# Kernel tuning notes

Measured on AMD Instinct MI355X. Metric: run time of the kernel, lower is better.

Reference implementation:

```python
import jax, jax.numpy as jnp
import numpy as np
import math

B, U, IN, H = 4096, 6, 256, 600
IKS, IVS, NIH = 64, 400, 1           # input attention key/value sizes, heads
CKS, CQS, NCH = 32, 32, 4            # comm attention key/query sizes, heads
CVS = H                              # comm value size forced to hidden_size
K = 4                                # top-k active units


@jax.custom_vjp
def blocked_grad(x, mask):
    return x

def _bg_fwd(x, mask):
    return x, mask

def _bg_bwd(mask, g):
    return (g * mask, jnp.zeros_like(mask))

blocked_grad.defvjp(_bg_fwd, _bg_bwd)


def _gll(x, w):
    # GroupLinearLayer: per-unit bmm, x (B,U,din) @ w (U,din,dout) -> (B,U,dout)
    return jnp.einsum('bud,udo->buo', x, w)


def setup_inputs() -> dict:
    key = jax.random.key(0)
    ks = jax.random.split(key, 16)
    r = lambda i, shape: (0.02 * jax.random.normal(ks[i], shape)).astype(jnp.float32)
    return dict(
        x=jax.random.normal(ks[0], (B, 1, IN), jnp.float32),
        hs=jax.random.normal(ks[1], (B, U, H), jnp.float32),
        Wk=r(2, (IN, NIH * IKS)), bk=jnp.zeros((NIH * IKS,), jnp.float32),
        Wv=r(3, (IN, NIH * IVS)), bv=jnp.zeros((NIH * IVS,), jnp.float32),
        Wq=r(4, (U, H, NIH * IKS)),
        x2h_w=r(5, (U, IVS, 3 * H)), h2h_w=r(6, (U, H, 3 * H)),
        Wq_=r(7, (U, H, NCH * CQS)), Wk_=r(8, (U, H, NCH * CKS)),
        Wv_=r(9, (U, H, NCH * CVS)), Wout=r(10, (U, NCH * CVS, CVS)),
    )


def reference(x, hs, Wk, bk, Wv, bv, Wq, x2h_w, h2h_w, Wq_, Wk_, Wv_, Wout):
    h_old = hs
    # append null input along dim 1 -> (B,2,IN)
    xcat = jnp.concatenate([x, jnp.zeros_like(x)], axis=1)
    # ---- input attention + top-k mask ----
    key_l = (xcat @ Wk + bk).reshape(B, 2, NIH, IKS).transpose(0, 2, 1, 3)   # (B,1,2,ks)
    val_l = (xcat @ Wv + bv).reshape(B, 2, NIH, IVS).mean(axis=2)             # (B,2,vs) mean over heads
    qry_l = _gll(hs, Wq).reshape(B, U, NIH, IKS).transpose(0, 2, 1, 3)        # (B,1,U,ks)
    scores = jnp.einsum('bhuk,bhnk->bhun', qry_l, key_l) / math.sqrt(IKS)
    scores = scores.mean(axis=1)                                               # (B,U,2)
    not_null = scores[:, :, 0]
    _, idx = jax.lax.top_k(not_null, K)                                        # (B,K)
    mask = jnp.zeros((B, U), jnp.float32).at[jnp.arange(B)[:, None], idx].set(1.0)
    probs = jax.nn.softmax(scores, axis=-1)                                    # dropout is identity (eval)
    inputs = jnp.einsum('bun,bnv->buv', probs, val_l) * mask[:, :, None]       # (B,U,vs)
    # ---- GroupGRU cell ----
    gx = _gll(inputs, x2h_w)
    gh = _gll(hs, h2h_w)
    i_r, i_i, i_n = jnp.split(gx, 3, axis=2)
    h_r, h_i, h_n = jnp.split(gh, 3, axis=2)
    rg = jax.nn.sigmoid(i_r + h_r)
    ig = jax.nn.sigmoid(i_i + h_i)
    ng = jnp.tanh(i_n + rg * h_n)
    hs = ng + ig * (hs - ng)
    # ---- communication attention (with blocked_grad) ----
    h_b = blocked_grad(hs, mask[:, :, None])
    q = _gll(h_b, Wq_).reshape(B, U, NCH, CQS).transpose(0, 2, 1, 3)   # (B,4,U,32)
    k = _gll(h_b, Wk_).reshape(B, U, NCH, CKS).transpose(0, 2, 1, 3)
    v = _gll(h_b, Wv_).reshape(B, U, NCH, CVS).transpose(0, 2, 1, 3)   # (B,4,U,600)
    att = jax.nn.softmax(jnp.einsum('bhuk,bhnk->bhun', q, k) / math.sqrt(CKS), axis=-1)
    att = att * mask[:, None, :, None]   # zero rows of inactive query units
    ctx = jnp.einsum('bhun,bhnv->bhuv', att, v).transpose(0, 2, 1, 3).reshape(B, U, NCH * CVS)
    ctx = _gll(ctx, Wout) + h_b
    m = mask[:, :, None]
    return m * ctx + (1.0 - m) * h_old
```

## Files before the change

kernel.cpp:

```cpp
#include <hip/hip_runtime.h>
#include <math.h>

typedef unsigned short u16;
typedef __attribute__((ext_vector_type(8))) short short8;
typedef __attribute__((ext_vector_type(4))) float f32x4;

constexpr int NB   = 4096;
constexpr int NU   = 6;
constexpr int NIN  = 256;
constexpr int NH   = 600;
constexpr int IKS  = 64;
constexpr int IVS  = 400;
constexpr int NCH  = 4;
constexpr int CVS  = 600;
constexpr int KTOP = 4;

constexpr int KVW  = IKS + IVS;
constexpr int QKW  = 256;
constexpr int VW   = NCH * CVS;

constexpr int KGRU = 1024;
constexpr int HOFS = 416;
constexpr int NGATE = 640;
constexpr int KH   = 640;
constexpr int VN   = 2432;
constexpr int BC   = 1024;
constexpr int NCHUNK = NB / BC;

constexpr long OFF_KV   = 0;
constexpr long OFF_QRY  = OFF_KV   + (long)NB * KVW;
constexpr long OFF_C0   = OFF_QRY  + (long)NB * NU * IKS;
constexpr long OFF_C1   = OFF_C0   + (long)NB * NU;
constexpr long OFF_MASK = OFF_C1   + (long)NB * NU;
constexpr long OFF_QK   = OFF_MASK + (long)NB * NU;
constexpr long OFF_ATTW = OFF_QK   + (long)NB * NU * QKW;
constexpr long OFF_HNBF = OFF_ATTW + (long)NB * NCH * NU * NU;
constexpr long OFF_WQK  = OFF_HNBF + (long)NU * NB * KH / 2;
constexpr long OFF_WV   = OFF_WQK  + (long)NU * QKW * KH / 2;
constexpr long OFF_WOUT = OFF_WV   + (long)NU * VN * KH / 2;
constexpr long OFF_WGRU = OFF_WOUT + (long)NU * NGATE * VN / 2;
constexpr long OFF_AGRU = OFF_WGRU + (long)NU * 3 * NGATE * KGRU / 2;
constexpr long OFF_VBUF = OFF_WGRU;
constexpr long OFF_CTXB = OFF_VBUF + (long)BC * NU * VN / 2;

__device__ __forceinline__ u16 f2bf(float f) {
    unsigned int x = __float_as_uint(f);
    x += 0x7FFFu + ((x >> 16) & 1u);
    return (u16)(x >> 16);
}
__device__ __forceinline__ float bf2f(u16 u) {
    return __uint_as_float(((unsigned int)u) << 16);
}
__device__ __forceinline__ void gl_lds16(const u16* g, u16* l) {
    __builtin_amdgcn_global_load_lds(
        (const __attribute__((address_space(1))) void*)g,
        (__attribute__((address_space(3))) void*)l, 16, 0, 0);
}

#define WAITVM_(N) asm volatile("s_waitcnt vmcnt(" #N ")" ::: "memory")
#define WAITVM(N)  WAITVM_(N)
#define WAITLG()   asm volatile("s_waitcnt lgkmcnt(0)" ::: "memory")
#define SBAR()     do { __builtin_amdgcn_sched_barrier(0); \
                        __builtin_amdgcn_s_barrier();      \
                        __builtin_amdgcn_sched_barrier(0); } while (0)

__global__ __launch_bounds__(256)
void wtrans_kernel(const float* __restrict__ src, long s_u, int s_ld, int s_colofs,
                   int Ksrc, int Nsub,
                   u16* __restrict__ dst, long d_u, int d_ld, int d_nofs, int d_kofs,
                   int gdiv, int s_gcol, int d_gnofs)
{
    __shared__ float tile[32][33];
    int z = blockIdx.z;
    int u = z, g = 0;
    if (gdiv > 1) { u = z / gdiv; g = z % gdiv; }
    const int k0 = blockIdx.x * 32, n0 = blockIdx.y * 32;
    const int t  = threadIdx.x;
    const int scol = s_colofs + g * s_gcol;
    const int dnof = d_nofs + g * d_gnofs;
    const float* S = src + (long)u * s_u;
    u16* D = dst + (long)u * d_u;
    #pragma unroll
    for (int r = 0; r < 4; r++) {
        int kk = r * 8 + (t >> 5), nn = t & 31;
        float v = 0.f;
        if (k0 + kk < Ksrc && n0 + nn < Nsub)
            v = S[(long)(k0 + kk) * s_ld + scol + n0 + nn];
        tile[kk][nn] = v;
    }
    __syncthreads();
    #pragma unroll
    for (int r = 0; r < 4; r++) {
        int nn = r * 8 + (t >> 5), kk = t & 31;
        if (n0 + nn < Nsub)
            D[(long)(dnof + n0 + nn) * d_ld + d_kofs + k0 + kk] = f2bf(tile[kk][nn]);
    }
}

__global__ __launch_bounds__(256)
void gemm_kv_kernel(const float* __restrict__ x,
                    const float* __restrict__ Wk, const float* __restrict__ bk,
                    const float* __restrict__ Wv, const float* __restrict__ bv,
                    float* __restrict__ kvout)
{
    const int m0 = blockIdx.x * 64;
    const int n0 = blockIdx.y * 64;
    const int tid = threadIdx.x;
    const int tm = tid / 16, tn = tid % 16;
    constexpr int K = NIN, N = KVW;

    __shared__ __align__(16) float As[32][72];
    __shared__ __align__(16) float Ws[32][68];
    float acc[4][4] = {};

    for (int k0 = 0; k0 < K; k0 += 32) {
        #pragma unroll
        for (int s2 = 0; s2 < 2; s2++) {
            int s = tid * 2 + s2;
            int row = s >> 3, kc = s & 7;
            float4 v = *(const float4*)&x[(long)(m0 + row) * K + k0 + kc * 4];
            As[kc*4+0][row] = v.x; As[kc*4+1][row] = v.y;
            As[kc*4+2][row] = v.z; As[kc*4+3][row] = v.w;
        }
        #pragma unroll
        for (int s2 = 0; s2 < 2; s2++) {
            int s = tid * 2 + s2;
            int kr = s >> 4, c4 = s & 15;
            int cg = n0 + c4 * 4;
            float4 v = {0,0,0,0};
            if (cg < IKS)    v = *(const float4*)&Wk[(long)(k0+kr)*IKS + cg];
            else if (cg < N) v = *(const float4*)&Wv[(long)(k0+kr)*IVS + (cg - IKS)];
            *(float4*)&Ws[kr][c4*4] = v;
        }
        __syncthreads();
        #pragma unroll
        for (int kk = 0; kk < 32; kk++) {
            float4 a4 = *(const float4*)&As[kk][tm*4];
            float4 w4 = *(const float4*)&Ws[kk][tn*4];
            float av[4] = {a4.x,a4.y,a4.z,a4.w}, wv[4] = {w4.x,w4.y,w4.z,w4.w};
            #pragma unroll
            for (int i = 0; i < 4; i++)
                #pragma unroll
                for (int j = 0; j < 4; j++)
                    acc[i][j] = fmaf(av[i], wv[j], acc[i][j]);
        }
        __syncthreads();
    }
    #pragma unroll
    for (int i = 0; i < 4; i++) {
        int row = m0 + tm*4 + i;
        #pragma unroll
        for (int j = 0; j < 4; j++) {
            int cg = n0 + tn*4 + j;
            if (cg < N) {
                float bias = (cg < IKS) ? bk[cg] : bv[cg - IKS];
                kvout[(long)row*N + cg] = acc[i][j] + bias;
            }
        }
    }
}

__global__ __launch_bounds__(256)
void gemm_qry_kernel(const float* __restrict__ A,
                     const float* __restrict__ W,
                     float* __restrict__ C)
{
    const int u  = blockIdx.z;
    const int m0 = blockIdx.x * 64;
    const int tid = threadIdx.x;
    const int tm = tid / 16, tn = tid % 16;
    constexpr int K = NH, N = IKS;
    const long lda = (long)NU * NH;

    __shared__ __align__(16) float As[32][72];
    __shared__ __align__(16) float Ws[32][68];
    const float* Au = A + (long)u * K;
    const float* Wu = W + (long)u * K * N;
    float acc[4][4] = {};

    for (int k0 = 0; k0 < K; k0 += 32) {
        #pragma unroll
        for (int s2 = 0; s2 < 2; s2++) {
            int s = tid * 2 + s2;
            int row = s >> 3, kc = s & 7;
            float4 v = {0,0,0,0};
            if (k0 + kc*4 < K)
                v = *(const float4*)&Au[(long)(m0 + row) * lda + k0 + kc * 4];
            As[kc*4+0][row] = v.x; As[kc*4+1][row] = v.y;
            As[kc*4+2][row] = v.z; As[kc*4+3][row] = v.w;
        }
        #pragma unroll
        for (int s2 = 0; s2 < 2; s2++) {
            int s = tid * 2 + s2;
            int kr = s >> 4, c4 = s & 15;
            float4 v = {0,0,0,0};
            if (k0 + kr < K)
                v = *(const float4*)&Wu[(long)(k0 + kr) * N + c4 * 4];
            *(float4*)&Ws[kr][c4*4] = v;
        }
        __syncthreads();
        #pragma unroll
        for (int kk = 0; kk < 32; kk++) {
            float4 a4 = *(const float4*)&As[kk][tm*4];
            float4 w4 = *(const float4*)&Ws[kk][tn*4];
            float av[4] = {a4.x,a4.y,a4.z,a4.w}, wv[4] = {w4.x,w4.y,w4.z,w4.w};
            #pragma unroll
            for (int i = 0; i < 4; i++)
                #pragma unroll
                for (int j = 0; j < 4; j++)
                    acc[i][j] = fmaf(av[i], wv[j], acc[i][j]);
        }
        __syncthreads();
    }
    #pragma unroll
    for (int i = 0; i < 4; i++) {
        int row = m0 + tm*4 + i;
        #pragma unroll
        for (int j = 0; j < 4; j++) {
            int c = tn*4 + j;
            C[(long)row*(NU*IKS) + (long)u*IKS + c] = acc[i][j];
        }
    }
}

__global__ __launch_bounds__(64)
void score_kernel(const float* __restrict__ qry, const float* __restrict__ kv,
                  const float* __restrict__ bk,
                  float* __restrict__ c0, float* __restrict__ c1,
                  float* __restrict__ maskf)
{
    const int b = blockIdx.x;
    const int t = threadIdx.x;
    __shared__ float s0s[NU], s1s[NU];

    float k0v = kv[(long)b*KVW + t];
    float bkv = bk[t];
    for (int u = 0; u < NU; u++) {
        float q  = qry[((long)b*NU + u)*IKS + t];
        float p0 = q * k0v, p1 = q * bkv;
        #pragma unroll
        for (int off = 32; off > 0; off >>= 1) {
            p0 += __shfl_down(p0, off);
            p1 += __shfl_down(p1, off);
        }
        if (t == 0) { s0s[u] = p0 * 0.125f; s1s[u] = p1 * 0.125f; }
    }
    __syncthreads();
    if (t < NU) {
        int u = t;
        float su = s0s[u];
        int rank = 0;
        #pragma unroll
        for (int j = 0; j < NU; j++) {
            float sj = s0s[j];
            if (sj > su || (sj == su && j < u)) rank++;
        }
        float m = (rank < KTOP) ? 1.0f : 0.0f;
        float a = s0s[u], bb = s1s[u];
        float mx = fmaxf(a, bb);
        float e0 = expf(a - mx), e1 = expf(bb - mx);
        float p0 = e0 / (e0 + e1);
        c0[(long)b*NU + u]    = m * p0;
        c1[(long)b*NU + u]    = m * (1.0f - p0);
        maskf[(long)b*NU + u] = m;
    }
}

__global__ __launch_bounds__(256)
void prep_gruA_kernel(const float* __restrict__ kv, const float* __restrict__ bv,
                      const float* __restrict__ hs,
                      const float* __restrict__ c0, const float* __restrict__ c1,
                      u16* __restrict__ Ag)
{
    long id = (long)blockIdx.x * 256 + threadIdx.x;
    const long total = (long)NU * NB * (KGRU / 8);
    if (id >= total) return;
    int k8 = (int)(id % (KGRU / 8));
    int b  = (int)((id / (KGRU / 8)) % NB);
    int u  = (int)(id / ((long)(KGRU / 8) * NB));
    int k  = k8 * 8;
    u16 o[8];
    if (k < IVS) {
        float cv0 = c0[(long)b*NU + u], cv1 = c1[(long)b*NU + u];
        const float* kp = kv + (long)b*KVW + IKS + k;
        const float* bp = bv + k;
        #pragma unroll
        for (int i = 0; i < 8; i++) o[i] = f2bf(cv0*kp[i] + cv1*bp[i]);
    } else if (k >= HOFS && k < HOFS + NH) {
        const float* hp = hs + ((long)b*NU + u)*NH + (k - HOFS);
        #pragma unroll
        for (int i = 0; i < 8; i++) o[i] = f2bf(hp[i]);
    } else {
        #pragma unroll
        for (int i = 0; i < 8; i++) o[i] = 0;
    }
    *(short8*)&Ag[id * 8] = *(const short8*)o;
}

__global__ __launch_bounds__(256, 3)
void gru_mfma_kernel(const u16* __restrict__ Ag, const u16* __restrict__ Wg,
                     const float* __restrict__ hs, u16* __restrict__ hnbf)
{
    const int u  = blockIdx.z;
    const int m0 = blockIdx.x * 128;
    const int n0 = blockIdx.y * 32;
    const int tid = threadIdx.x;
    const int wid = tid >> 6, lane = tid & 63;
    const int wm = wid >> 1, wn = wid & 1;
    const int lrow = lane & 15, lkq = lane >> 4;
    const int srow = lane >> 2;
    const int scs  = (((lane & 3) ^ ((lane >> 3) & 3)) * 8);
    const int cofs = ((lkq ^ ((lrow >> 1) & 3)) * 8);

    __shared__ __align__(16) u16 As[3][128 * 32];
    __shared__ __align__(16) u16 Bs[3][128 * 32];

    const u16* Au = Ag + (long)u * NB * KGRU;
    const u16* Wu = Wg + (long)u * 3 * NGATE * KGRU;

    f32x4 aR[4], aI[4], aNX[4], aNH[4];
    #pragma unroll
    for (int m = 0; m < 4; m++) {
        aR[m] = (f32x4){0,0,0,0}; aI[m] = (f32x4){0,0,0,0};
        aNX[m] = (f32x4){0,0,0,0}; aNH[m] = (f32x4){0,0,0,0};
    }

#define GSTAGE(BUF, T) do {                                                   \
        const long kk0 = (long)(T) * 32;                                      \
        _Pragma("unroll")                                                     \
        for (int i2 = 0; i2 < 2; i2++) {                                      \
            int R = wid*32 + i2*16;                                           \
            int row = R + srow;                                               \
            gl_lds16(Au + (long)(m0 + row)*KGRU + kk0 + scs,                  \
                     &As[BUF][R * 32]);                                       \
            int g = row >> 5; if (g > 2) g = 2;     \
            int rn = row & 31;                                                \
            gl_lds16(Wu + ((long)g*NGATE + n0 + rn)*KGRU + kk0 + scs,         \
                     &Bs[BUF][R * 32]);                                       \
        }                                                                     \
    } while (0)

#define GCOMPUTE(BUF, T) do {                                                 \
        __builtin_amdgcn_s_setprio(1);                                        \
        short8 af[4], bR, bI, bN;                                             \
        _Pragma("unroll")                                                     \
        for (int m = 0; m < 4; m++)                                           \
            af[m] = *(const short8*)&As[BUF][(wm*64 + m*16 + lrow)*32 + cofs];\
        {                                                                     \
            int nr = wn*16 + lrow;                                            \
            bR = *(const short8*)&Bs[BUF][(0*32 + nr)*32 + cofs];             \
            bI = *(const short8*)&Bs[BUF][(1*32 + nr)*32 + cofs];             \
            bN = *(const short8*)&Bs[BUF][(2*32 + nr)*32 + cofs];             \
        }                                                                     \
        _Pragma("unroll")                                                     \
        for (int m = 0; m < 4; m++) {                                         \
            aR[m] = __builtin_amdgcn_mfma_f32_16x16x32_bf16(af[m], bR, aR[m], 0, 0, 0); \
            aI[m] = __builtin_amdgcn_mfma_f32_16x16x32_bf16(af[m], bI, aI[m], 0, 0, 0); \
        }                                                                     \
        if ((T) < HOFS/32) {                                                  \
            _Pragma("unroll")                                                 \
            for (int m = 0; m < 4; m++)                                       \
                aNX[m] = __builtin_amdgcn_mfma_f32_16x16x32_bf16(af[m], bN, aNX[m], 0, 0, 0); \
        } else {                                                              \
            _Pragma("unroll")                                                 \
            for (int m = 0; m < 4; m++)                                       \
                aNH[m] = __builtin_amdgcn_mfma_f32_16x16x32_bf16(af[m], bN, aNH[m], 0, 0, 0); \
        }                                                                     \
        __builtin_amdgcn_s_setprio(0);                                        \
    } while (0)

    constexpr int KSTEPS = KGRU / 32;
    GSTAGE(0, 0);
    int bc = 0, bn = 1;
    for (int t = 0; t < KSTEPS - 1; ++t) {
        GSTAGE(bn, t + 1);
        WAITVM(4); SBAR();
        GCOMPUTE(bc, t);
        bc = bn; bn = (bn == 2) ? 0 : bn + 1;
    }
    WAITVM(0); SBAR();
    GCOMPUTE(bc, KSTEPS - 1);
#undef GCOMPUTE
#undef GSTAGE

    #pragma unroll
    for (int m = 0; m < 4; m++) {
        #pragma unroll
        for (int r = 0; r < 4; r++) {
            int row = m0 + wm*64 + m*16 + lkq*4 + r;
            int col = n0 + wn*16 + lrow;
            u16 ov = 0;
            if (col < NH) {
                float rg = 1.0f / (1.0f + expf(-aR[m][r]));
                float ig = 1.0f / (1.0f + expf(-aI[m][r]));
                float ng = tanhf(aNX[m][r] + rg * aNH[m][r]);
                float h  = hs[((long)row*NU + u)*NH + col];
                ov = f2bf(ng + ig * (h - ng));
            }
            hnbf[(long)u*NB*KH + (long)row*KH + col] = ov;
        }
    }
}

template<int EPI>
__global__ __launch_bounds__(256, 2)
void mfgemm_kernel(const u16* __restrict__ A, long sAu, int lda,
                   const u16* __restrict__ Bw, long sBu, int ldb,
                   float* __restrict__ Cf, u16* __restrict__ C16,
                   long sCu, int ldc, int ksteps,
                   const float* __restrict__ maskf,
                   const u16* __restrict__ hnbf,
                   const float* __restrict__ hs,
                   int bbase)
{
    const int u  = blockIdx.z;
    const int m0 = blockIdx.x * 128;
    const int n0 = blockIdx.y * 128;
    const int tid = threadIdx.x;
    const int wid = tid >> 6, lane = tid & 63;
    const int wm = wid >> 1, wn = wid & 1;
    const int lrow = lane & 15, lkq = lane >> 4;
    const int l8 = lane & 7, lr8 = lane >> 3;
    const int rsw = lrow & 7;

    __shared__ __align__(16) u16 As[2][128 * 64];
    __shared__ __align__(16) u16 Bs[2][128 * 64];

    const u16* Au = A + (long)u * sAu;
    const u16* Bu = Bw + (long)u * sBu;

    f32x4 acc[4][4];
    #pragma unroll
    for (int m = 0; m < 4; m++)
        #pragma unroll
        for (int n = 0; n < 4; n++) acc[m][n] = (f32x4){0,0,0,0};

#define MSTAGE(BUF, KS) do {                                                  \
        const long kk0 = (long)(KS) * 64;                                     \
        _Pragma("unroll")                                                     \
        for (int i2 = 0; i2 < 4; i2++) {                                      \
            int rw = i2*32 + wid*8 + lr8;                                     \
            int co = ((l8 ^ (rw & 7)) * 8);                                   \
            gl_lds16(Au + (long)(m0 + rw)*lda + kk0 + co,                     \
                     &As[BUF][(i2*32 + wid*8) * 64]);                         \
            gl_lds16(Bu + (long)(n0 + rw)*ldb + kk0 + co,                     \
                     &Bs[BUF][(i2*32 + wid*8) * 64]);                         \
        }                                                                     \
    } while (0)

#define MCOMPUTE(BUF) do {                                                    \
        __builtin_amdgcn_s_setprio(1);                                        \
        _Pragma("unroll")                                                     \
        for (int ks2 = 0; ks2 < 2; ks2++) {                                   \
            const int cofs = (((ks2*4 + lkq) ^ rsw) * 8);                     \
            short8 af[4], bfr[4];                                             \
            _Pragma("unroll")                                                 \
            for (int m = 0; m < 4; m++)                                       \
                af[m] = *(const short8*)&As[BUF][(wm*64 + m*16 + lrow)*64 + cofs]; \
            _Pragma("unroll")                                                 \
            for (int n = 0; n < 4; n++)                                       \
                bfr[n] = *(const short8*)&Bs[BUF][(wn*64 + n*16 + lrow)*64 + cofs]; \
            _Pragma("unroll")                                                 \
            for (int m = 0; m < 4; m++)                                       \
                _Pragma("unroll")                                             \
                for (int n = 0; n < 4; n++)                                   \
                    acc[m][n] = __builtin_amdgcn_mfma_f32_16x16x32_bf16(af[m], bfr[n], acc[m][n], 0, 0, 0); \
        }                                                                     \
        __builtin_amdgcn_s_setprio(0);                                        \
    } while (0)

#define MPH(BUF, T, W) do {                                                   \
        if ((T) + 1 < ksteps) MSTAGE((BUF)^1, (T)+1);                         \
        WAITVM(W); SBAR();                                                    \
        MCOMPUTE(BUF);                                                        \
        WAITLG(); SBAR();                                                     \
    } while (0)

    MSTAGE(0, 0);
    int t = 0;
    for (; t + 2 < ksteps; t += 2) { MPH(0, t, 8); MPH(1, t+1, 8); }
    if (t + 2 == ksteps) { MPH(0, t, 8); MPH(1, t+1, 0); }
    else                 { MPH(0, t, 0); }
#undef MPH
#undef MCOMPUTE
#undef MSTAGE

    #pragma unroll
    for (int m = 0; m < 4; m++) {
        #pragma unroll
        for (int r = 0; r < 4; r++) {
            int row = m0 + wm*64 + m*16 + lkq*4 + r;
            #pragma unroll
            for (int n = 0; n < 4; n++) {
                int col = n0 + wn*64 + n*16 + lrow;
                float v = acc[m][n][r];
                if (EPI == 0) {
                    Cf[(long)u*sCu + (long)row*ldc + col] = v;
                } else if (EPI == 2) {
                    C16[(long)u*sCu + (long)row*ldc + col] = f2bf(v);
                } else {
                    if (col < NH) {
                        int b = bbase + row;
                        long o = ((long)b*NU + u)*NH + col;
                        float mk = maskf[(long)b*NU + u];
                        float hv = bf2f(hnbf[(long)u*NB*KH + (long)b*KH + col]);
                        Cf[o] = (mk > 0.5f) ? (v + hv) : hs[o];
                    }
                }
            }
        }
    }
}

__global__ __launch_bounds__(64)
void attw_kernel(const float* __restrict__ qk, const float* __restrict__ maskf,
                 float* __restrict__ attw)
{
    const int bh = blockIdx.x;
    const int b = bh / NCH, h = bh % NCH;
    const int t = threadIdx.x;
    __shared__ float lg[NU][NU];

    if (t < NU * NU) {
        int uq = t / NU, un = t % NU;
        const float* qp = qk + ((long)b*NU + uq)*QKW + h*32;
        const float* kp = qk + ((long)b*NU + un)*QKW + 128 + h*32;
        float s = 0;
        #pragma unroll
        for (int i = 0; i < 32; i++) s = fmaf(qp[i], kp[i], s);
        lg[uq][un] = s * 0.17677669529663687f;
    }
    __syncthreads();
    if (t < NU) {
        int uq = t;
        float mx = -1e30f;
        #pragma unroll
        for (int n = 0; n < NU; n++) mx = fmaxf(mx, lg[uq][n]);
        float e[NU], se = 0;
        #pragma unroll
        for (int n = 0; n < NU; n++) { e[n] = expf(lg[uq][n] - mx); se += e[n]; }
        float m = maskf[(long)b*NU + uq];
        float inv = m / se;
        #pragma unroll
        for (int n = 0; n < NU; n++)
            attw[(((long)b*NCH + h)*NU + uq)*NU + n] = e[n] * inv;
    }
}

__global__ __launch_bounds__(256)
void ctx2_kernel(const float* __restrict__ attw, const u16* __restrict__ v16,
                 u16* __restrict__ ctx16, int bbase)
{
    __shared__ float att_s[32][NCH * NU * NU];
    const int c0 = blockIdx.x * 64;
    const int b0 = blockIdx.y * 32;
    const int tid = threadIdx.x;

    for (int i = tid; i < 32 * 144; i += 256) {
        int bl = i / 144, j = i % 144;
        att_s[bl][j] = attw[(long)(bbase + b0 + bl) * 144 + j];
    }
    __syncthreads();

    const int bl = tid >> 3;
    const int c  = c0 + (tid & 7) * 8;
    const long rowbase = (long)(b0 + bl) * NU;

    if (c >= VW) {
        short8 z = {0,0,0,0,0,0,0,0};
        #pragma unroll
        for (int u = 0; u < NU; u++)
            *(short8*)&ctx16[(rowbase + u) * VN + c] = z;
        return;
    }
    const int h = c / CVS;
    const float* aw = &att_s[bl][h * 36];

    float acc[NU][8] = {};
    #pragma unroll
    for (int n = 0; n < NU; n++) {
        short8 vv = *(const short8*)&v16[(rowbase + n) * VN + c];
        float vf[8];
        #pragma unroll
        for (int i = 0; i < 8; i++) vf[i] = bf2f((u16)vv[i]);
        #pragma unroll
        for (int u = 0; u < NU; u++) {
            float a = aw[u * 6 + n];
            #pragma unroll
            for (int i = 0; i < 8; i++) acc[u][i] = fmaf(a, vf[i], acc[u][i]);
        }
    }
    #pragma unroll
    for (int u = 0; u < NU; u++) {
        short8 o;
        #pragma unroll
        for (int i = 0; i < 8; i++) o[i] = (short)f2bf(acc[u][i]);
        *(short8*)&ctx16[(rowbase + u) * VN + c] = o;
    }
}

extern "C" void kernel_launch(void* const* d_in, const int* in_sizes, int n_in,
                              void* d_out, int out_size, void* d_ws, size_t ws_size,
                              hipStream_t stream)
{
    const float* x    = (const float*)d_in[0];
    const float* hs   = (const float*)d_in[1];
    const float* Wk   = (const float*)d_in[2];
    const float* bk   = (const float*)d_in[3];
    const float* Wv   = (const float*)d_in[4];
    const float* bv   = (const float*)d_in[5];
    const float* Wq   = (const float*)d_in[6];
    const float* x2h  = (const float*)d_in[7];
    const float* h2h  = (const float*)d_in[8];
    const float* Wq_  = (const float*)d_in[9];
    const float* Wk_  = (const float*)d_in[10];
    const float* Wv_  = (const float*)d_in[11];
    const float* Wout = (const float*)d_in[12];
    float* out = (float*)d_out;
    float* ws  = (float*)d_ws;

    float* kv    = ws + OFF_KV;
    float* qry   = ws + OFF_QRY;
    float* c0b   = ws + OFF_C0;
    float* c1b   = ws + OFF_C1;
    float* maskf = ws + OFF_MASK;
    float* qk    = ws + OFF_QK;
    float* attw  = ws + OFF_ATTW;
    u16*   hnbf  = (u16*)(ws + OFF_HNBF);
    u16*   wqk   = (u16*)(ws + OFF_WQK);
    u16*   wv    = (u16*)(ws + OFF_WV);
    u16*   wout  = (u16*)(ws + OFF_WOUT);
    u16*   wgru  = (u16*)(ws + OFF_WGRU);
    u16*   agru  = (u16*)(ws + OFF_AGRU);
    u16*   vbuf16 = (u16*)(ws + OFF_VBUF);
    u16*   ctx16  = (u16*)(ws + OFF_CTXB);

    wtrans_kernel<<<dim3(20, 4, NU), 256, 0, stream>>>(
        Wq_, (long)NH*128, 128, 0, NH, 128, wqk, (long)QKW*KH, KH, 0, 0, 1, 0, 0);
    wtrans_kernel<<<dim3(20, 4, NU), 256, 0, stream>>>(
        Wk_, (long)NH*128, 128, 0, NH, 128, wqk, (long)QKW*KH, KH, 128, 0, 1, 0, 0);
    wtrans_kernel<<<dim3(20, 75, NU), 256, 0, stream>>>(
        Wv_, (long)NH*VW, VW, 0, NH, VW, wv, (long)VN*KH, KH, 0, 0, 1, 0, 0);
    wtrans_kernel<<<dim3(76, 19, NU), 256, 0, stream>>>(
        Wout, (long)VW*NH, NH, 0, VW, NH, wout, (long)NGATE*VN, VN, 0, 0, 1, 0, 0);
    wtrans_kernel<<<dim3(13, 19, NU*3), 256, 0, stream>>>(
        x2h, (long)IVS*3*NH, 3*NH, 0, IVS, NH,
        wgru, (long)3*NGATE*KGRU, KGRU, 0, 0, 3, NH, NGATE);
    wtrans_kernel<<<dim3(19, 19, NU*3), 256, 0, stream>>>(
        h2h, (long)NH*3*NH, 3*NH, 0, NH, NH,
        wgru, (long)3*NGATE*KGRU, KGRU, 0, HOFS, 3, NH, NGATE);

    gemm_kv_kernel<<<dim3(NB/64, (KVW+63)/64), 256, 0, stream>>>(x, Wk, bk, Wv, bv, kv);
    gemm_qry_kernel<<<dim3(NB/64, 1, NU), 256, 0, stream>>>(hs, Wq, qry);
    score_kernel<<<NB, 64, 0, stream>>>(qry, kv, bk, c0b, c1b, maskf);

    {
        long total = (long)NU * NB * (KGRU/8);
        prep_gruA_kernel<<<(unsigned)((total + 255)/256), 256, 0, stream>>>(
            kv, bv, hs, c0b, c1b, agru);
    }
    gru_mfma_kernel<<<dim3(NB/128, NGATE/32, NU), 256, 0, stream>>>(agru, wgru, hs, hnbf);

    mfgemm_kernel<0><<<dim3(NB/128, QKW/128, NU), 256, 0, stream>>>(
        hnbf, (long)NB*KH, KH, wqk, (long)QKW*KH, KH,
        qk, nullptr, (long)QKW, NU*QKW, KH/64, nullptr, nullptr, nullptr, 0);
    attw_kernel<<<NB*NCH, 64, 0, stream>>>(qk, maskf, attw);

    for (int ch = 0; ch < NCHUNK; ch++) {
        mfgemm_kernel<2><<<dim3(BC/128, VN/128, NU), 256, 0, stream>>>(
            hnbf + (long)ch*BC*KH, (long)NB*KH, KH, wv, (long)VN*KH, KH,
            nullptr, vbuf16, (long)VN, NU*VN, KH/64, nullptr, nullptr, nullptr, 0);
        ctx2_kernel<<<dim3(VN/64, BC/32), 256, 0, stream>>>(
            attw, vbuf16, ctx16, ch*BC);
        mfgemm_kernel<1><<<dim3(BC/128, NGATE/128, NU), 256, 0, stream>>>(
            ctx16, (long)VN, NU*VN, wout, (long)NGATE*VN, VN,
            out, nullptr, 0, 0, VN/64, maskf, hnbf, hs, ch*BC);
    }
}
```

Before: 848.9 us.

## Compute ctx in place over V buffer, double chunk size, add XCD block swizzle

The ctx2 kernel now reads all six V rows of a column slice into registers and writes the attention-weighted context back into the same buffer. This removes the separate ctx buffer and frees workspace, which lets the batch chunk grow from 1024 to 2048 so there are fewer chunk iterations and larger GEMM grids. The GRU and MFMA GEMM kernels also remap block IDs so that consecutive tiles land on the same XCD, which should improve L2 reuse. In-place aliasing is safe only because each thread reads all of its inputs before writing, and the larger chunk must still fit in the workspace.

After: 707.8 us. 16.6% less time.

```diff
diff --git a/kernel.cpp b/kernel.cpp
--- a/kernel.cpp
+++ b/kernel.cpp
@@ -24,7 +24,7 @@
 constexpr int NGATE = 640;
 constexpr int KH   = 640;
 constexpr int VN   = 2432;
-constexpr int BC   = 1024;
+constexpr int BC   = 2048;
 constexpr int NCHUNK = NB / BC;
 
 constexpr long OFF_KV   = 0;
@@ -41,7 +41,6 @@
 constexpr long OFF_WGRU = OFF_WOUT + (long)NU * NGATE * VN / 2;
 constexpr long OFF_AGRU = OFF_WGRU + (long)NU * 3 * NGATE * KGRU / 2;
 constexpr long OFF_VBUF = OFF_WGRU;
-constexpr long OFF_CTXB = OFF_VBUF + (long)BC * NU * VN / 2;
 
 __device__ __forceinline__ u16 f2bf(float f) {
     unsigned int x = __float_as_uint(f);
@@ -55,6 +54,17 @@
     __builtin_amdgcn_global_load_lds(
         (const __attribute__((address_space(1))) void*)g,
         (__attribute__((address_space(3))) void*)l, 16, 0, 0);
+}
+__device__ __forceinline__ void xcd_swz(int& bx, int& by, int& bz)
+{
+    const int gx = gridDim.x, gy = gridDim.y, gz = gridDim.z;
+    const int n = gx * gy * gz;
+    if (n & 7) return;
+    int lid = bx + gx * (by + gy * bz);
+    const int q = n >> 3;
+    int w = (lid & 7) * q + (lid >> 3);
+    bx = w % gx; int rest = w / gx;
+    by = rest % gy; bz = rest / gy;
 }
 
 #define WAITVM_(N) asm volatile("s_waitcnt vmcnt(" #N ")" ::: "memory")
@@ -301,9 +311,11 @@
 void gru_mfma_kernel(const u16* __restrict__ Ag, const u16* __restrict__ Wg,
                      const float* __restrict__ hs, u16* __restrict__ hnbf)
 {
-    const int u  = blockIdx.z;
-    const int m0 = blockIdx.x * 128;
-    const int n0 = blockIdx.y * 32;
+    int bx = blockIdx.x, by = blockIdx.y, bz = blockIdx.z;
+    xcd_swz(bx, by, bz);
+    const int u  = bz;
+    const int m0 = bx * 128;
+    const int n0 = by * 32;
     const int tid = threadIdx.x;
     const int wid = tid >> 6, lane = tid & 63;
     const int wm = wid >> 1, wn = wid & 1;
@@ -413,9 +425,11 @@
                    const float* __restrict__ hs,
                    int bbase)
 {
-    const int u  = blockIdx.z;
-    const int m0 = blockIdx.x * 128;
-    const int n0 = blockIdx.y * 128;
+    int bx = blockIdx.x, by = blockIdx.y, bz = blockIdx.z;
+    xcd_swz(bx, by, bz);
+    const int u  = bz;
+    const int m0 = bx * 128;
+    const int n0 = by * 128;
     const int tid = threadIdx.x;
     const int wid = tid >> 6, lane = tid & 63;
     const int wm = wid >> 1, wn = wid & 1;
@@ -548,8 +562,7 @@
 }
 
 __global__ __launch_bounds__(256)
-void ctx2_kernel(const float* __restrict__ attw, const u16* __restrict__ v16,
-                 u16* __restrict__ ctx16, int bbase)
+void ctx2_kernel(const float* __restrict__ attw, u16* vc, int bbase)
 {
     __shared__ float att_s[32][NCH * NU * NU];
     const int c0 = blockIdx.x * 64;
@@ -570,32 +583,32 @@
         short8 z = {0,0,0,0,0,0,0,0};
         #pragma unroll
         for (int u = 0; u < NU; u++)
-            *(short8*)&ctx16[(rowbase + u) * VN + c] = z;
+            *(short8*)&vc[(rowbase + u) * VN + c] = z;
         return;
     }
     const int h = c / CVS;
     const float* aw = &att_s[bl][h * 36];
 
-    float acc[NU][8] = {};
+    float vf[NU][8];
     #pragma unroll
     for (int n = 0; n < NU; n++) {
-        short8 vv = *(const short8*)&v16[(rowbase + n) * VN + c];
-        float vf[8];
-        #pragma unroll
-        for (int i = 0; i < 8; i++) vf[i] = bf2f((u16)vv[i]);
-        #pragma unroll
-        for (int u = 0; u < NU; u++) {
+        short8 vv = *(const short8*)&vc[(rowbase + n) * VN + c];
+        #pragma unroll
+        for (int i = 0; i < 8; i++) vf[n][i] = bf2f((u16)vv[i]);
+    }
+    #pragma unroll
+    for (int u = 0; u < NU; u++) {
+        float acc[8] = {};
+        #pragma unroll
+        for (int n = 0; n < NU; n++) {
             float a = aw[u * 6 + n];
             #pragma unroll
-            for (int i = 0; i < 8; i++) acc[u][i] = fmaf(a, vf[i], acc[u][i]);
-        }
-    }
-    #pragma unroll
-    for (int u = 0; u < NU; u++) {
+            for (int i = 0; i < 8; i++) acc[i] = fmaf(a, vf[n][i], acc[i]);
+        }
         short8 o;
         #pragma unroll
-        for (int i = 0; i < 8; i++) o[i] = (short)f2bf(acc[u][i]);
-        *(short8*)&ctx16[(rowbase + u) * VN + c] = o;
+        for (int i = 0; i < 8; i++) o[i] = (short)f2bf(acc[i]);
+        *(short8*)&vc[(rowbase + u) * VN + c] = o;
     }
 }
 
@@ -632,8 +645,7 @@
     u16*   wout  = (u16*)(ws + OFF_WOUT);
     u16*   wgru  = (u16*)(ws + OFF_WGRU);
     u16*   agru  = (u16*)(ws + OFF_AGRU);
-    u16*   vbuf16 = (u16*)(ws + OFF_VBUF);
-    u16*   ctx16  = (u16*)(ws + OFF_CTXB);
+    u16*   vcbuf = (u16*)(ws + OFF_VBUF);
 
     wtrans_kernel<<<dim3(20, 4, NU), 256, 0, stream>>>(
         Wq_, (long)NH*128, 128, 0, NH, 128, wqk, (long)QKW*KH, KH, 0, 0, 1, 0, 0);
@@ -669,11 +681,11 @@
     for (int ch = 0; ch < NCHUNK; ch++) {
         mfgemm_kernel<2><<<dim3(BC/128, VN/128, NU), 256, 0, stream>>>(
             hnbf + (long)ch*BC*KH, (long)NB*KH, KH, wv, (long)VN*KH, KH,
-            nullptr, vbuf16, (long)VN, NU*VN, KH/64, nullptr, nullptr, nullptr, 0);
+            nullptr, vcbuf, (long)VN, NU*VN, KH/64, nullptr, nullptr, nullptr, 0);
         ctx2_kernel<<<dim3(VN/64, BC/32), 256, 0, stream>>>(
-            attw, vbuf16, ctx16, ch*BC);
+            attw, vcbuf, ch*BC);
         mfgemm_kernel<1><<<dim3(BC/128, NGATE/128, NU), 256, 0, stream>>>(
-            ctx16, (long)VN, NU*VN, wout, (long)NGATE*VN, VN,
+            vcbuf, (long)VN, NU*VN, wout, (long)NGATE*VN, VN,
             out, nullptr, 0, 0, VN/64, maskf, hnbf, hs, ch*BC);
     }
 }
```
